# Kernel optimization log

Measured on AMD Instinct MI355X. Metric: run time of the kernel, lower is better.

Reference implementation:

```python
import jax, jax.numpy as jnp
import numpy as np

N_NODES = 100000
N_EDGES = 3200000
N_HID = 3
HEAD_OUT = 1024


def setup_inputs() -> dict:
    key = jax.random.key(0)
    ks = jax.random.split(key, 8)
    feat1 = jax.random.normal(ks[0], (N_NODES, 1), dtype=jnp.float32)
    feat2 = jax.random.normal(ks[1], (N_NODES, 1), dtype=jnp.float32)
    norm = jax.random.uniform(ks[2], (N_EDGES,), dtype=jnp.float32)
    src = jax.random.randint(ks[3], (N_EDGES,), 0, N_NODES, dtype=jnp.int32)
    dst = jax.random.randint(ks[4], (N_EDGES,), 0, N_NODES, dtype=jnp.int32)
    # per-layer GIN apply_func Linear(1,1): weight [n_hid,1,1], bias [n_hid,1]
    gin_w = jax.random.normal(ks[5], (N_HID, 1, 1), dtype=jnp.float32)
    gin_b = jax.random.normal(ks[6], (N_HID, 1), dtype=jnp.float32) * 0.1
    # head Linear(num_nodes, 1024), stored as [in, out]
    net_w = jax.random.normal(ks[7], (N_NODES, HEAD_OUT), dtype=jnp.float32) * (1.0 / np.sqrt(N_NODES))
    net_b = jnp.zeros((HEAD_OUT,), dtype=jnp.float32)
    return {"feat1": feat1, "feat2": feat2, "norm": norm, "src": src, "dst": dst,
            "gin_w": gin_w, "gin_b": gin_b, "net_w": net_w, "net_b": net_b}


def reference(feat1, feat2, norm, src, dst, gin_w, gin_b, net_w, net_b):
    n = feat1.shape[0]
    e_dtype = feat1.dtype
    # in-degree (same every layer); DGL mean over mailbox divides by in-degree
    deg = jax.ops.segment_sum(jnp.ones((src.shape[0],), e_dtype), dst, num_segments=n)
    inv_deg = (1.0 / jnp.maximum(deg, 1.0))[:, None]  # [N,1]

    def forward_each(feat):
        x = feat  # [N,1]
        saved = []
        for l in range(gin_w.shape[0]):
            msg = x[src] * norm[:, None]                                # gather + edge weight [E,1]
            agg = jax.ops.segment_sum(msg, dst, num_segments=n) * inv_deg  # mean aggregate [N,1]
            rst = (x + agg) @ gin_w[l].T + gin_b[l]                     # GIN: (1+eps)*x + agg, eps=0, then Linear
            saved.append(rst)                                           # forward hook captures pre-relu output
            x = jax.nn.relu(rst)
        feats = jnp.mean(jnp.stack(saved), axis=0)  # mean over layers [N,1]
        h = feats.reshape(1, -1)                    # flatten -> [1, N]
        return h @ net_w + net_b                    # [1, 1024]

    x1 = forward_each(feat1)
    x2 = forward_each(feat2)
    return jax.nn.sigmoid(jnp.sum(x1 * x2, axis=1, keepdims=True))  # [1,1]
```

## Files before the change

### kernel.cpp

```cpp
#include <hip/hip_runtime.h>
#include <math.h>

static constexpr int NN  = 100000;
static constexpr int NE  = 3200000;
static constexpr int HO  = 1024;
static constexpr int BSH = 5;
static constexpr int BMASK = 31;
static constexpr int NB  = 3125;
static constexpr int NBP = NB + 1;
static constexpr int PB  = 256;
static constexpr int AT  = 512;
static constexpr int CHUNK = NE / PB;
static constexpr int PER_A = (NB + AT - 1) / AT;
static constexpr int RPB = 50;
static constexpr int HB  = NN / RPB;
static constexpr int CAP = 2048;
static constexpr int BT  = 49;
static constexpr int BSTRIDE = 1536;

typedef float f4v __attribute__((ext_vector_type(4)));

__device__ __forceinline__ int bucket_swz(int blk) {
    int x = blk & 7, g = blk >> 3;
    return (x < 5) ? x * 391 + g : 1955 + (x - 5) * 390 + g;
}

__global__ __launch_bounds__(AT) void partA_k(const float* __restrict__ f1,
                                              const float* __restrict__ f2,
                                              const int* __restrict__ src,
                                              const int* __restrict__ dst,
                                              const float* __restrict__ norm,
                                              int* __restrict__ loffg,
                                              uint2* __restrict__ blocked,
                                              float2* __restrict__ x0,
                                              float* __restrict__ xacc) {
    __shared__ int hist[NB];
    __shared__ int wt[8];
    int blk = blockIdx.x, t = threadIdx.x;
    int lane = t & 63, w = t >> 6;
    int gi = blk * AT + t;
    if (gi < NN) x0[gi] = make_float2(f1[gi], f2[gi]);
    if (blk == 0) {
        for (int i = t; i < 2 * HO; i += AT) xacc[i] = 0.f;
    }
    for (int i = t; i < NB; i += AT) hist[i] = 0;
    __syncthreads();
    int base = blk * CHUNK;
    for (int i = t; i < CHUNK; i += AT)
        atomicAdd(&hist[dst[base + i] >> BSH], 1);
    __syncthreads();
    int loc[PER_A]; int s = 0;
    int b0 = t * PER_A;
#pragma unroll
    for (int k = 0; k < PER_A; ++k) {
        int i = b0 + k;
        int v = (i < NB) ? hist[i] : 0;
        loc[k] = s; s += v;
    }
    int incl = s;
#pragma unroll
    for (int off = 1; off < 64; off <<= 1) {
        int v = __shfl_up(incl, off, 64);
        if (lane >= off) incl += v;
    }
    if (lane == 63) wt[w] = incl;
    __syncthreads();
    int wpre = 0;
#pragma unroll
    for (int k = 0; k < 8; ++k) if (k < w) wpre += wt[k];
    int carry = wpre + incl - s;
#pragma unroll
    for (int k = 0; k < PER_A; ++k) {
        int i = b0 + k;
        if (i < NB) {
            int e = carry + loc[k];
            loffg[blk * NBP + i] = e;
            hist[i] = e;
        }
    }
    __syncthreads();
    for (int i = t; i < CHUNK; i += AT) {
        int e = base + i;
        int d = dst[e];
        int pos = atomicAdd(&hist[d >> BSH], 1);
        blocked[base + pos] = make_uint2((unsigned)src[e] | ((unsigned)(d & BMASK) << 17),
                                         __float_as_uint(norm[e]));
    }
}

__global__ __launch_bounds__(256) void transT_k(const int* __restrict__ loffg,
                                                int* __restrict__ loffT) {
    __shared__ int tile[64][65];
    int bx = blockIdx.x % BT;
    int ky = blockIdx.x / BT;
    int tx = threadIdx.x & 63, ty = threadIdx.x >> 6;
    int b = bx * 64 + tx;
#pragma unroll
    for (int j = 0; j < 16; ++j) {
        int k = ky * 64 + ty + j * 4;
        tile[ty + j * 4][tx] = (b < NB) ? loffg[k * NBP + b] : 0;
    }
    __syncthreads();
#pragma unroll
    for (int j = 0; j < 16; ++j) {
        int row = ty + j * 4;
        int bb = bx * 64 + row;
        if (bb < NB) loffT[(size_t)bb * PB + ky * 64 + tx] = tile[tx][row];
    }
}

__global__ __launch_bounds__(256) void sortB_k(const uint2* __restrict__ blocked,
                                               const int* __restrict__ loffT,
                                               unsigned* __restrict__ s2out,
                                               int2* __restrict__ noff) {
    __shared__ uint2 rec[CAP];
    __shared__ int wtot[4];
    __shared__ int cnt[32], curs[32];
    __shared__ float inv[32];
    int t = threadIdx.x;
    int lane = t & 63, w = t >> 6;
    int b = bucket_swz(blockIdx.x);
    int gbase = b * BSTRIDE;
    int o0 = loffT[(size_t)b * PB + t];
    int o1 = (b == NB - 1) ? CHUNK : loffT[(size_t)(b + 1) * PB + t];
    int len = o1 - o0;
    if (t < 32) cnt[t] = 0;
    int incl = len;
#pragma unroll
    for (int off = 1; off < 64; off <<= 1) {
        int v = __shfl_up(incl, off, 64);
        if (lane >= off) incl += v;
    }
    if (lane == 63) wtot[w] = incl;
    __syncthreads();
    int wpre = 0, total = 0;
#pragma unroll
    for (int k = 0; k < 4; ++k) {
        int tv = wtot[k];
        if (k < w) wpre += tv;
        total += tv;
    }
    int start = wpre + incl - len;
    if (total > CAP) total = CAP;
    {
        int lm = (len > 0) ? len - 1 : 0;
        int o0c = (o0 < CHUNK - 1) ? o0 : CHUNK - 1;
        const uint2* srcq = blocked + (size_t)t * CHUNK + o0c;
        uint2 q0 = srcq[0];
        uint2 q1 = srcq[lm < 1 ? lm : 1];
        uint2 q2 = srcq[lm < 2 ? lm : 2];
        uint2 q3 = srcq[lm < 3 ? lm : 3];
        uint2 q4 = srcq[lm < 4 ? lm : 4];
        uint2 q5 = srcq[lm < 5 ? lm : 5];
        uint2 q6 = srcq[lm < 6 ? lm : 6];
        uint2 q7 = srcq[lm < 7 ? lm : 7];
        if (len > 0 && start + 0 < CAP) rec[start + 0] = q0;
        if (len > 1 && start + 1 < CAP) rec[start + 1] = q1;
        if (len > 2 && start + 2 < CAP) rec[start + 2] = q2;
        if (len > 3 && start + 3 < CAP) rec[start + 3] = q3;
        if (len > 4 && start + 4 < CAP) rec[start + 4] = q4;
        if (len > 5 && start + 5 < CAP) rec[start + 5] = q5;
        if (len > 6 && start + 6 < CAP) rec[start + 6] = q6;
        if (len > 7 && start + 7 < CAP) rec[start + 7] = q7;
        for (int j = 8; j < len; ++j)
            if (start + j < CAP) rec[start + j] = srcq[j];
    }
    __syncthreads();
    for (int i = t; i < total; i += 256)
        atomicAdd(&cnt[(rec[i].x >> 17) & BMASK], 1);
    __syncthreads();
    if (t < 32) {
        int c = cnt[t];
        int c4 = (c + 3) & ~3;
        int ic4 = c4;
#pragma unroll
        for (int off = 1; off < 32; off <<= 1) {
            int v = __shfl_up(ic4, off, 32);
            if (t >= off) ic4 += v;
        }
        int pre4 = ic4 - c4;
        curs[t] = pre4;
        inv[t] = 1.0f / fmaxf((float)c, 1.0f);
        noff[(b << BSH) + t] = make_int2(gbase + pre4, gbase + pre4 + c4);
        for (int j = c; j < c4; ++j) s2out[gbase + pre4 + j] = 0u;
    }
    __syncthreads();
    for (int i = t; i < total; i += 256) {
        uint2 r = rec[i];
        int lo = (r.x >> 17) & BMASK;
        int pos = atomicAdd(&curs[lo], 1);
        float v = __uint_as_float(r.y) * inv[lo];
        int q = (int)(v * 32768.f + 0.5f);
        if (q > 32767) q = 32767;
        s2out[gbase + pos] = (r.x & 131071u) | ((unsigned)q << 17);
    }
}

template<int L0>
__global__ __launch_bounds__(256) void layer_k(const unsigned* __restrict__ s2,
                                               const int2* __restrict__ noff,
                                               const float2* __restrict__ xin,
                                               float2* __restrict__ xout,
                                               float2* __restrict__ ssum,
                                               const float* __restrict__ gw,
                                               const float* __restrict__ gb, int l) {
    int gid = blockIdx.x * 256 + threadIdx.x;
    int node = gid >> 3, r = gid & 7;
    if (node >= NN) return;
    int2 no = noff[node];
    int i0 = no.x, i1 = no.y;
    float ax = 0.f, ay = 0.f;
    const float qs = 1.0f / 32768.0f;
    for (int i = i0 + 4 * r; i < i1; i += 32) {
        uint4 q = *reinterpret_cast<const uint4*>(s2 + i);
        float2 xa = xin[q.x & 131071u]; float wa = (float)(q.x >> 17) * qs;
        float2 xb = xin[q.y & 131071u]; float wb = (float)(q.y >> 17) * qs;
        float2 xc = xin[q.z & 131071u]; float wc = (float)(q.z >> 17) * qs;
        float2 xd = xin[q.w & 131071u]; float wd = (float)(q.w >> 17) * qs;
        ax = fmaf(xa.x, wa, ax); ay = fmaf(xa.y, wa, ay);
        ax = fmaf(xb.x, wb, ax); ay = fmaf(xb.y, wb, ay);
        ax = fmaf(xc.x, wc, ax); ay = fmaf(xc.y, wc, ay);
        ax = fmaf(xd.x, wd, ax); ay = fmaf(xd.y, wd, ay);
    }
#pragma unroll
    for (int off = 1; off < 8; off <<= 1) {
        ax += __shfl_xor(ax, off, 64);
        ay += __shfl_xor(ay, off, 64);
    }
    if (r == 0) {
        float wv = gw[l], bb = gb[l];
        float2 xv = xin[node];
        float rx = fmaf(xv.x + ax, wv, bb);
        float ry = fmaf(xv.y + ay, wv, bb);
        if (L0) ssum[node] = make_float2(rx, ry);
        else { float2 s = ssum[node]; ssum[node] = make_float2(s.x + rx, s.y + ry); }
        xout[node] = make_float2(fmaxf(rx, 0.f), fmaxf(ry, 0.f));
    }
}

__global__ __launch_bounds__(256) void head_k(const float2* __restrict__ ssum,
                                              const float* __restrict__ W,
                                              float* __restrict__ part) {
    __shared__ float sf0[RPB], sf1[RPB];
    int r0 = blockIdx.x * RPB;
    int t = threadIdx.x;
    const float sc = 1.0f / 3.0f;
    if (t < RPB) {
        float2 s = ssum[r0 + t];
        sf0[t] = s.x * sc;
        sf1[t] = s.y * sc;
    }
    __syncthreads();
    float ax1=0.f, ay1=0.f, az1=0.f, aw1=0.f;
    float ax2=0.f, ay2=0.f, az2=0.f, aw2=0.f;
    int j0 = t * 4;
    const f4v* Wp = reinterpret_cast<const f4v*>(W + (size_t)r0 * HO + j0);
#pragma unroll 5
    for (int k = 0; k < RPB; ++k) {
        f4v w4 = __builtin_nontemporal_load(Wp);
        Wp += HO / 4;
        float v1 = sf0[k], v2 = sf1[k];
        ax1 = fmaf(v1, w4.x, ax1); ay1 = fmaf(v1, w4.y, ay1);
        az1 = fmaf(v1, w4.z, az1); aw1 = fmaf(v1, w4.w, aw1);
        ax2 = fmaf(v2, w4.x, ax2); ay2 = fmaf(v2, w4.y, ay2);
        az2 = fmaf(v2, w4.z, az2); aw2 = fmaf(v2, w4.w, aw2);
    }
    float* pp = part + (size_t)blockIdx.x * 2048;
    pp[j0]   = ax1; pp[j0+1] = ay1; pp[j0+2] = az1; pp[j0+3] = aw1;
    pp[1024+j0]   = ax2; pp[1024+j0+1] = ay2;
    pp[1024+j0+2] = az2; pp[1024+j0+3] = aw2;
}

__global__ __launch_bounds__(256) void reduce_k(const float* __restrict__ part,
                                                float* __restrict__ xacc) {
    int gid = blockIdx.x * 256 + threadIdx.x;
    int j = gid & 2047;
    int seg = gid >> 11;
    int b0 = (seg * HB) >> 5, b1 = ((seg + 1) * HB) >> 5;
    float s = 0.f;
    for (int b = b0; b < b1; ++b) s += part[(size_t)b * 2048 + j];
    atomicAdd(&xacc[j], s);
}

__global__ void final_k(const float* __restrict__ xacc, const float* __restrict__ nb,
                        float* __restrict__ out) {
    __shared__ float red[256];
    int t = threadIdx.x;
    float v = 0.f;
    for (int j = t; j < HO; j += 256)
        v += (xacc[j] + nb[j]) * (xacc[HO + j] + nb[j]);
    red[t] = v;
    __syncthreads();
    for (int s = 128; s > 0; s >>= 1) {
        if (t < s) red[t] += red[t + s];
        __syncthreads();
    }
    if (t == 0) out[0] = 1.0f / (1.0f + expf(-red[0]));
}

extern "C" void kernel_launch(void* const* d_in, const int* in_sizes, int n_in,
                              void* d_out, int out_size, void* d_ws, size_t ws_size,
                              hipStream_t stream) {
    const float* feat1 = (const float*)d_in[0];
    const float* feat2 = (const float*)d_in[1];
    const float* norm  = (const float*)d_in[2];
    const int*   src   = (const int*)  d_in[3];
    const int*   dst   = (const int*)  d_in[4];
    const float* gin_w = (const float*)d_in[5];
    const float* gin_b = (const float*)d_in[6];
    const float* net_w = (const float*)d_in[7];
    const float* net_b = (const float*)d_in[8];
    float* out = (float*)d_out;

    char* p = (char*)d_ws;
    uint2* blocked   = (uint2*)p;             p += (size_t)NE * 8;
    float* part      = (float*)blocked;
    unsigned* sorted2 = (unsigned*)p;         p += (size_t)NB * BSTRIDE * 4;
    int*   loffg     = (int*)p;               p += (size_t)PB * NBP * 4;
    int*   loffT     = (int*)p;               p += (size_t)NB * PB * 4;
    int2*  noff      = (int2*)p;              p += (size_t)NN * 8;
    float2* x0       = (float2*)p;            p += (size_t)NN * 8;
    float2* x1       = (float2*)p;            p += (size_t)NN * 8;
    float2* ssum     = (float2*)p;            p += (size_t)NN * 8;
    float* xacc      = (float*)p;             p += (size_t)2 * HO * 4;

    int lg = (NN * 8 + 255) / 256;

    partA_k<<<PB, AT, 0, stream>>>(feat1, feat2, src, dst, norm, loffg, blocked,
                                   x0, xacc);
    transT_k<<<BT * 4, 256, 0, stream>>>(loffg, loffT);
    sortB_k<<<NB, 256, 0, stream>>>(blocked, loffT, sorted2, noff);

    layer_k<1><<<lg, 256, 0, stream>>>(sorted2, noff, x0, x1, ssum, gin_w, gin_b, 0);
    layer_k<0><<<lg, 256, 0, stream>>>(sorted2, noff, x1, x0, ssum, gin_w, gin_b, 1);
    layer_k<0><<<lg, 256, 0, stream>>>(sorted2, noff, x0, x1, ssum, gin_w, gin_b, 2);

    head_k<<<HB, 256, 0, stream>>>(ssum, net_w, part);
    reduce_k<<<256, 256, 0, stream>>>(part, xacc);
    final_k<<<1, 256, 0, stream>>>(xacc, net_b, out);
}
```

Measured before the change: 219.0 us.

## Fuse first GIN layer into sort, drop transpose and final kernels

Removes the transpose kernel by having sortB read the per-block offsets strided straight from loffg. The first GIN layer is computed inside sortB from the just-sorted edges kept in shared memory, which saves one launch and a global re-read of the sorted edge list. The final sigmoid/dot reduction moves into the last block of reduce_k using an atomic ticket counter. The costs are uncoalesced strided offset loads in sortB, more shared memory per block, and a threadfence-based last-block pattern.

```diff
diff --git a/kernel.cpp b/kernel.cpp
--- a/kernel.cpp
+++ b/kernel.cpp
@@ -15,7 +15,6 @@
 static constexpr int RPB = 50;
 static constexpr int HB  = NN / RPB;
 static constexpr int CAP = 2048;
-static constexpr int BT  = 49;
 static constexpr int BSTRIDE = 1536;
 
 typedef float f4v __attribute__((ext_vector_type(4)));
@@ -33,7 +32,8 @@
                                               int* __restrict__ loffg,
                                               uint2* __restrict__ blocked,
                                               float2* __restrict__ x0,
-                                              float* __restrict__ xacc) {
+                                              float* __restrict__ xacc,
+                                              int* __restrict__ done) {
     __shared__ int hist[NB];
     __shared__ int wt[8];
     int blk = blockIdx.x, t = threadIdx.x;
@@ -42,6 +42,7 @@
     if (gi < NN) x0[gi] = make_float2(f1[gi], f2[gi]);
     if (blk == 0) {
         for (int i = t; i < 2 * HO; i += AT) xacc[i] = 0.f;
+        if (t == 0) *done = 0;
     }
     for (int i = t; i < NB; i += AT) hist[i] = 0;
     __syncthreads();
@@ -88,41 +89,26 @@
     }
 }
 
-__global__ __launch_bounds__(256) void transT_k(const int* __restrict__ loffg,
-                                                int* __restrict__ loffT) {
-    __shared__ int tile[64][65];
-    int bx = blockIdx.x % BT;
-    int ky = blockIdx.x / BT;
-    int tx = threadIdx.x & 63, ty = threadIdx.x >> 6;
-    int b = bx * 64 + tx;
-#pragma unroll
-    for (int j = 0; j < 16; ++j) {
-        int k = ky * 64 + ty + j * 4;
-        tile[ty + j * 4][tx] = (b < NB) ? loffg[k * NBP + b] : 0;
-    }
-    __syncthreads();
-#pragma unroll
-    for (int j = 0; j < 16; ++j) {
-        int row = ty + j * 4;
-        int bb = bx * 64 + row;
-        if (bb < NB) loffT[(size_t)bb * PB + ky * 64 + tx] = tile[tx][row];
-    }
-}
-
 __global__ __launch_bounds__(256) void sortB_k(const uint2* __restrict__ blocked,
-                                               const int* __restrict__ loffT,
+                                               const int* __restrict__ loffg,
                                                unsigned* __restrict__ s2out,
-                                               int2* __restrict__ noff) {
-    __shared__ uint2 rec[CAP];
+                                               int2* __restrict__ noff,
+                                               const float2* __restrict__ x0,
+                                               float2* __restrict__ x1,
+                                               float2* __restrict__ ssum,
+                                               const float* __restrict__ gw,
+                                               const float* __restrict__ gb) {
+    __shared__ __align__(16) uint2 rec[CAP];
+    __shared__ __align__(16) unsigned ol[CAP];
     __shared__ int wtot[4];
-    __shared__ int cnt[32], curs[32];
+    __shared__ int cnt[32], curs[32], pre4s[32], c4s[32];
     __shared__ float inv[32];
     int t = threadIdx.x;
     int lane = t & 63, w = t >> 6;
     int b = bucket_swz(blockIdx.x);
     int gbase = b * BSTRIDE;
-    int o0 = loffT[(size_t)b * PB + t];
-    int o1 = (b == NB - 1) ? CHUNK : loffT[(size_t)(b + 1) * PB + t];
+    int o0 = loffg[t * NBP + b];
+    int o1 = (b == NB - 1) ? CHUNK : loffg[t * NBP + b + 1];
     int len = o1 - o0;
     if (t < 32) cnt[t] = 0;
     int incl = len;
@@ -180,9 +166,13 @@
         }
         int pre4 = ic4 - c4;
         curs[t] = pre4;
+        pre4s[t] = pre4; c4s[t] = c4;
         inv[t] = 1.0f / fmaxf((float)c, 1.0f);
         noff[(b << BSH) + t] = make_int2(gbase + pre4, gbase + pre4 + c4);
-        for (int j = c; j < c4; ++j) s2out[gbase + pre4 + j] = 0u;
+        for (int j = c; j < c4; ++j) {
+            s2out[gbase + pre4 + j] = 0u;
+            ol[pre4 + j] = 0u;
+        }
     }
     __syncthreads();
     for (int i = t; i < total; i += 256) {
@@ -192,11 +182,44 @@
         float v = __uint_as_float(r.y) * inv[lo];
         int q = (int)(v * 32768.f + 0.5f);
         if (q > 32767) q = 32767;
-        s2out[gbase + pos] = (r.x & 131071u) | ((unsigned)q << 17);
-    }
-}
-
-template<int L0>
+        unsigned rr = (r.x & 131071u) | ((unsigned)q << 17);
+        s2out[gbase + pos] = rr;
+        ol[pos] = rr;
+    }
+    __syncthreads();
+    {
+        int lo = t >> 3, r = t & 7;
+        int p0 = pre4s[lo], c4 = c4s[lo];
+        float ax = 0.f, ay = 0.f;
+        const float qs = 1.0f / 32768.0f;
+        for (int i = p0 + 4 * r; i < p0 + c4; i += 32) {
+            uint4 q = *reinterpret_cast<const uint4*>(&ol[i]);
+            float2 xa = x0[q.x & 131071u]; float wa = (float)(q.x >> 17) * qs;
+            float2 xb = x0[q.y & 131071u]; float wb = (float)(q.y >> 17) * qs;
+            float2 xc = x0[q.z & 131071u]; float wc = (float)(q.z >> 17) * qs;
+            float2 xd = x0[q.w & 131071u]; float wd = (float)(q.w >> 17) * qs;
+            ax = fmaf(xa.x, wa, ax); ay = fmaf(xa.y, wa, ay);
+            ax = fmaf(xb.x, wb, ax); ay = fmaf(xb.y, wb, ay);
+            ax = fmaf(xc.x, wc, ax); ay = fmaf(xc.y, wc, ay);
+            ax = fmaf(xd.x, wd, ax); ay = fmaf(xd.y, wd, ay);
+        }
+#pragma unroll
+        for (int off = 1; off < 8; off <<= 1) {
+            ax += __shfl_xor(ax, off, 64);
+            ay += __shfl_xor(ay, off, 64);
+        }
+        if (r == 0) {
+            int node = (b << BSH) + lo;
+            float wv = gw[0], bb = gb[0];
+            float2 xv = x0[node];
+            float rx = fmaf(xv.x + ax, wv, bb);
+            float ry = fmaf(xv.y + ay, wv, bb);
+            ssum[node] = make_float2(rx, ry);
+            x1[node] = make_float2(fmaxf(rx, 0.f), fmaxf(ry, 0.f));
+        }
+    }
+}
+
 __global__ __launch_bounds__(256) void layer_k(const unsigned* __restrict__ s2,
                                                const int2* __restrict__ noff,
                                                const float2* __restrict__ xin,
@@ -232,8 +255,8 @@
         float2 xv = xin[node];
         float rx = fmaf(xv.x + ax, wv, bb);
         float ry = fmaf(xv.y + ay, wv, bb);
-        if (L0) ssum[node] = make_float2(rx, ry);
-        else { float2 s = ssum[node]; ssum[node] = make_float2(s.x + rx, s.y + ry); }
+        float2 s = ssum[node];
+        ssum[node] = make_float2(s.x + rx, s.y + ry);
         xout[node] = make_float2(fmaxf(rx, 0.f), fmaxf(ry, 0.f));
     }
 }
@@ -272,7 +295,10 @@
 }
 
 __global__ __launch_bounds__(256) void reduce_k(const float* __restrict__ part,
-                                                float* __restrict__ xacc) {
+                                                float* __restrict__ xacc,
+                                                const float* __restrict__ nb,
+                                                float* __restrict__ out,
+                                                int* __restrict__ done) {
     int gid = blockIdx.x * 256 + threadIdx.x;
     int j = gid & 2047;
     int seg = gid >> 11;
@@ -280,22 +306,26 @@
     float s = 0.f;
     for (int b = b0; b < b1; ++b) s += part[(size_t)b * 2048 + j];
     atomicAdd(&xacc[j], s);
-}
-
-__global__ void final_k(const float* __restrict__ xacc, const float* __restrict__ nb,
-                        float* __restrict__ out) {
-    __shared__ float red[256];
-    int t = threadIdx.x;
-    float v = 0.f;
-    for (int j = t; j < HO; j += 256)
-        v += (xacc[j] + nb[j]) * (xacc[HO + j] + nb[j]);
-    red[t] = v;
-    __syncthreads();
-    for (int s = 128; s > 0; s >>= 1) {
-        if (t < s) red[t] += red[t + s];
+    __threadfence();
+    __syncthreads();
+    __shared__ int ticket;
+    if (threadIdx.x == 0) ticket = atomicAdd(done, 1);
+    __syncthreads();
+    if (ticket == 255) {
+        __threadfence();
+        int t = threadIdx.x;
+        float v = 0.f;
+        for (int jj = t; jj < HO; jj += 256)
+            v += (xacc[jj] + nb[jj]) * (xacc[HO + jj] + nb[jj]);
+        __shared__ float red[256];
+        red[t] = v;
         __syncthreads();
-    }
-    if (t == 0) out[0] = 1.0f / (1.0f + expf(-red[0]));
+        for (int st = 128; st > 0; st >>= 1) {
+            if (t < st) red[t] += red[t + st];
+            __syncthreads();
+        }
+        if (t == 0) out[0] = 1.0f / (1.0f + expf(-red[0]));
+    }
 }
 
 extern "C" void kernel_launch(void* const* d_in, const int* in_sizes, int n_in,
@@ -317,25 +347,21 @@
     float* part      = (float*)blocked;
     unsigned* sorted2 = (unsigned*)p;         p += (size_t)NB * BSTRIDE * 4;
     int*   loffg     = (int*)p;               p += (size_t)PB * NBP * 4;
-    int*   loffT     = (int*)p;               p += (size_t)NB * PB * 4;
     int2*  noff      = (int2*)p;              p += (size_t)NN * 8;
     float2* x0       = (float2*)p;            p += (size_t)NN * 8;
     float2* x1       = (float2*)p;            p += (size_t)NN * 8;
     float2* ssum     = (float2*)p;            p += (size_t)NN * 8;
     float* xacc      = (float*)p;             p += (size_t)2 * HO * 4;
+    int*   done      = (int*)p;               p += 16;
 
     int lg = (NN * 8 + 255) / 256;
 
     partA_k<<<PB, AT, 0, stream>>>(feat1, feat2, src, dst, norm, loffg, blocked,
-                                   x0, xacc);
-    transT_k<<<BT * 4, 256, 0, stream>>>(loffg, loffT);
-    sortB_k<<<NB, 256, 0, stream>>>(blocked, loffT, sorted2, noff);
-
-    layer_k<1><<<lg, 256, 0, stream>>>(sorted2, noff, x0, x1, ssum, gin_w, gin_b, 0);
-    layer_k<0><<<lg, 256, 0, stream>>>(sorted2, noff, x1, x0, ssum, gin_w, gin_b, 1);
-    layer_k<0><<<lg, 256, 0, stream>>>(sorted2, noff, x0, x1, ssum, gin_w, gin_b, 2);
-
+                                   x0, xacc, done);
+    sortB_k<<<NB, 256, 0, stream>>>(blocked, loffg, sorted2, noff,
+                                    x0, x1, ssum, gin_w, gin_b);
+    layer_k<<<lg, 256, 0, stream>>>(sorted2, noff, x1, x0, ssum, gin_w, gin_b, 1);
+    layer_k<<<lg, 256, 0, stream>>>(sorted2, noff, x0, x1, ssum, gin_w, gin_b, 2);
     head_k<<<HB, 256, 0, stream>>>(ssum, net_w, part);
-    reduce_k<<<256, 256, 0, stream>>>(part, xacc);
-    final_k<<<1, 256, 0, stream>>>(xacc, net_b, out);
-}
+    reduce_k<<<256, 256, 0, stream>>>(part, xacc, net_b, out, done);
+}
```

After: 229.2 us. 4.7% more time.
